# Performance work log

Measured on AMD Instinct MI355X. Metric: run time of the kernel, lower is better.

## Reference

```python
import jax, jax.numpy as jnp
import numpy as np

NHEAD = 16
EPS = 1e-5


def layer_norm(x, w, b):
    mu = jnp.mean(x, axis=-1, keepdims=True)
    var = jnp.var(x, axis=-1, keepdims=True)
    return (x - mu) * jax.lax.rsqrt(var + EPS) * w + b


def setup_inputs() -> dict:
    key = jax.random.key(0)
    ks = jax.random.split(key, 14)
    B, S, E, F = 16, 1024, 1024, 4096
    s = 0.02
    return {
        "x": jax.random.normal(ks[0], (B, S, E), jnp.float32),
        "in_proj_w": jax.random.normal(ks[1], (3 * E, E), jnp.float32) * s,
        "in_proj_b": jax.random.normal(ks[2], (3 * E,), jnp.float32) * s,
        "out_w": jax.random.normal(ks[3], (E, E), jnp.float32) * s,
        "out_b": jax.random.normal(ks[4], (E,), jnp.float32) * s,
        "lin1_w": jax.random.normal(ks[5], (F, E), jnp.float32) * s,
        "lin1_b": jax.random.normal(ks[6], (F,), jnp.float32) * s,
        "lin2_w": jax.random.normal(ks[7], (E, F), jnp.float32) * s,
        "lin2_b": jax.random.normal(ks[8], (E,), jnp.float32) * s,
        "norm1_w": jnp.ones((E,), jnp.float32),
        "norm1_b": jnp.zeros((E,), jnp.float32),
        "norm2_w": jnp.ones((E,), jnp.float32),
        "norm2_b": jnp.zeros((E,), jnp.float32),
    }


def reference(x, in_proj_w, in_proj_b, out_w, out_b, lin1_w, lin1_b, lin2_w, lin2_b,
              norm1_w, norm1_b, norm2_w, norm2_b):
    B, S, E = x.shape
    H = NHEAD
    D = E // H

    # --- pre-norm self-attention (q = k = v = norm1(x)) ---
    xn = layer_norm(x, norm1_w, norm1_b)
    qkv = xn @ in_proj_w.T + in_proj_b                      # [B,S,3E]
    q, k, v = jnp.split(qkv, 3, axis=-1)
    q = q.reshape(B, S, H, D)
    k = k.reshape(B, S, H, D)
    v = v.reshape(B, S, H, D)
    scale = 1.0 / jnp.sqrt(jnp.asarray(D, x.dtype))
    scores = jnp.einsum("bqhd,bkhd->bhqk", q, k) * scale    # [B,H,S,S]
    attn = jax.nn.softmax(scores, axis=-1)
    ctx = jnp.einsum("bhqk,bkhd->bqhd", attn, v).reshape(B, S, E)
    attn_out = ctx @ out_w.T + out_b
    x = x + attn_out

    # --- pre-norm feedforward (gelu) ---
    xn2 = layer_norm(x, norm2_w, norm2_b)
    h = jax.nn.gelu(xn2 @ lin1_w.T + lin1_b, approximate=False)
    x = x + (h @ lin2_w.T + lin2_b)
    return x
```

## Files before the change

kernel.cpp:

```cpp
#include <hip/hip_runtime.h>


typedef __attribute__((ext_vector_type(8))) short bf16x8;
typedef __attribute__((ext_vector_type(4))) float f32x4;
typedef __attribute__((ext_vector_type(8))) unsigned short u16x8;
typedef __attribute__((ext_vector_type(4))) unsigned short u16x4;

__device__ __forceinline__ float bf2f(unsigned short u) {
    return __uint_as_float(((unsigned int)u) << 16);
}
__device__ __forceinline__ unsigned short f2bf(float f) {
    unsigned int u = __float_as_uint(f);
    u += 0x7fffu + ((u >> 16) & 1u);
    return (unsigned short)(u >> 16);
}
__device__ __forceinline__ unsigned int pkbf_trunc(float a, float b) {
    return (__float_as_uint(a) >> 16) | (__float_as_uint(b) & 0xffff0000u);
}

__device__ __forceinline__ void gload_lds16(const unsigned short* g, unsigned short* l) {
    __builtin_amdgcn_global_load_lds(
        (const __attribute__((address_space(1))) unsigned int*)g,
        (__attribute__((address_space(3))) unsigned int*)l, 16, 0, 0);
}

#define FENCE() asm volatile("" ::: "memory")
#define BAR()                         \
    do {                              \
        FENCE();                      \
        __builtin_amdgcn_s_barrier(); \
        FENCE();                      \
    } while (0)
#define VMCNT(n)                                               \
    do {                                                       \
        asm volatile("s_waitcnt vmcnt(" #n ")" ::: "memory");  \
        __builtin_amdgcn_sched_barrier(0);                     \
    } while (0)

__global__ __launch_bounds__(256) void cvt_kernel(const float* __restrict__ in,
                                                  unsigned short* __restrict__ out, int n4) {
    int i = blockIdx.x * 256 + threadIdx.x;
    if (i >= n4) return;
    float4 v = ((const float4*)in)[i];
    u16x4 o;
    o[0] = f2bf(v.x); o[1] = f2bf(v.y); o[2] = f2bf(v.z); o[3] = f2bf(v.w);
    ((u16x4*)out)[i] = o;
}

__global__ __launch_bounds__(256) void ln_kernel(const float* __restrict__ x,
                                                 const float* __restrict__ w,
                                                 const float* __restrict__ b,
                                                 unsigned short* __restrict__ out) {
    const int row = blockIdx.x;
    const int t = threadIdx.x;
    const float* xr = x + (size_t)row * 1024;
    float4 v = *(const float4*)(xr + t * 4);
    float s = v.x + v.y + v.z + v.w;
    float sq = v.x * v.x + v.y * v.y + v.z * v.z + v.w * v.w;
#pragma unroll
    for (int off = 32; off > 0; off >>= 1) {
        s += __shfl_xor(s, off);
        sq += __shfl_xor(sq, off);
    }
    __shared__ float rs_[4], rq_[4];
    if ((t & 63) == 0) { rs_[t >> 6] = s; rq_[t >> 6] = sq; }
    __syncthreads();
    s = rs_[0] + rs_[1] + rs_[2] + rs_[3];
    sq = rq_[0] + rq_[1] + rq_[2] + rq_[3];
    const float mu = s * (1.0f / 1024.0f);
    const float var = sq * (1.0f / 1024.0f) - mu * mu;
    const float rstd = rsqrtf(var + 1e-5f);
    const int c = t * 4;
    float4 wv = *(const float4*)(w + c);
    float4 bv = *(const float4*)(b + c);
    u16x4 o;
    o[0] = f2bf((v.x - mu) * rstd * wv.x + bv.x);
    o[1] = f2bf((v.y - mu) * rstd * wv.y + bv.y);
    o[2] = f2bf((v.z - mu) * rstd * wv.z + bv.z);
    o[3] = f2bf((v.w - mu) * rstd * wv.w + bv.w);
    *(u16x4*)(out + (size_t)row * 1024 + c) = o;
}

template <int EPI>
__global__ __launch_bounds__(512, 2) void gemm_bt(const unsigned short* __restrict__ A,
                                                  const unsigned short* __restrict__ Bt,
                                                  const float* __restrict__ bias,
                                                  const float* __restrict__ resid,
                                                  void* __restrict__ outp,
                                                  int M, int N, int K) {
    __shared__ __align__(16) unsigned short sA[2][256 * 64];
    __shared__ __align__(16) unsigned short sB[2][256 * 64];
    const int t = threadIdx.x;
    const int lane = t & 63;
    const int w = t >> 6;
    const int wm = w >> 2;
    const int wn = w & 3;
    const int quad = lane >> 4;
    const int cl = lane & 15;

    const int nwg = gridDim.x * gridDim.y;
    int wg = blockIdx.y * gridDim.x + blockIdx.x;
    wg = (wg & 7) * (nwg >> 3) + (wg >> 3);
    const int mBase = (wg / gridDim.x) * 256;
    const int nBase = (wg % gridDim.x) * 256;

    const int rl = lane >> 3;
    const int ch = ((lane & 7) ^ rl) * 8;
    const unsigned short* gA = A + (size_t)mBase * K;
    const unsigned short* gB = Bt + (size_t)nBase * K;

#define STAGE_A(buf, hf, k0)                                                          \
    do {                                                                              \
        _Pragma("unroll") for (int u_ = 0; u_ < 2; ++u_) {                            \
            const int r_ = (hf) * 128 + (w * 2 + u_) * 8;                             \
            gload_lds16(gA + (size_t)(r_ + rl) * K + (k0) + ch, &sA[buf][r_ * 64]);   \
        }                                                                             \
    } while (0)
#define STAGE_B(buf, hf, k0)                                                          \
    do {                                                                              \
        _Pragma("unroll") for (int u_ = 0; u_ < 2; ++u_) {                            \
            const int r_ = (hf) * 128 + (w * 2 + u_) * 8;                             \
            gload_lds16(gB + (size_t)(r_ + rl) * K + (k0) + ch, &sB[buf][r_ * 64]);   \
        }                                                                             \
    } while (0)
#define READ_B8(buf)                                                                  \
    do {                                                                              \
        _Pragma("unroll") for (int nf_ = 0; nf_ < 4; ++nf_) {                         \
            const int rb_ = wn * 64 + nf_ * 16 + cl;                                  \
            _Pragma("unroll") for (int ks_ = 0; ks_ < 2; ++ks_)                       \
                bf[nf_][ks_] = *(const bf16x8*)(&sB[buf][rb_ * 64 +                   \
                                     (((quad + 4 * ks_) ^ (rb_ & 7)) * 8)]);          \
        }                                                                             \
    } while (0)
#define READ_A2(buf, mfb)                                                             \
    do {                                                                              \
        _Pragma("unroll") for (int m_ = 0; m_ < 2; ++m_) {                            \
            const int ra_ = wm * 128 + ((mfb) + m_) * 16 + cl;                        \
            _Pragma("unroll") for (int ks_ = 0; ks_ < 2; ++ks_)                       \
                af[m_][ks_] = *(const bf16x8*)(&sA[buf][ra_ * 64 +                    \
                                     (((quad + 4 * ks_) ^ (ra_ & 7)) * 8)]);          \
        }                                                                             \
    } while (0)
#define MFMA_Q(q)                                                                     \
    do {                                                                              \
        __builtin_amdgcn_s_setprio(1);                                                \
        _Pragma("unroll") for (int m_ = 0; m_ < 2; ++m_)                              \
            _Pragma("unroll") for (int nf_ = 0; nf_ < 4; ++nf_)                       \
                _Pragma("unroll") for (int ks_ = 0; ks_ < 2; ++ks_)                   \
                    acc[2 * (q) + m_][nf_] = __builtin_amdgcn_mfma_f32_16x16x32_bf16( \
                        af[m_][ks_], bf[nf_][ks_], acc[2 * (q) + m_][nf_], 0, 0, 0);  \
        __builtin_amdgcn_s_setprio(0);                                                \
    } while (0)

    f32x4 acc[8][4] = {};
    bf16x8 bf[4][2];
    bf16x8 af[2][2];

    STAGE_A(0, 0, 0); STAGE_A(0, 1, 0);
    STAGE_B(0, 0, 0); STAGE_B(0, 1, 0);
    STAGE_B(1, 0, 64); STAGE_B(1, 1, 64);
    VMCNT(4);
    BAR();

    const int NI = K >> 7;
    for (int i = 0; i < NI; ++i) {
        const bool more = (i + 1 < NI);
        const int kT1 = (i << 7) + 64;
        const int kN = (i + 1) << 7;
        READ_B8(0); READ_A2(0, 0);
        STAGE_A(1, 0, kT1);
        BAR(); MFMA_Q(0); BAR();
        READ_A2(0, 2);
        STAGE_A(1, 1, kT1);
        BAR(); MFMA_Q(1); BAR();
        READ_A2(0, 4);
        if (more) STAGE_B(0, 0, kN);
        BAR(); MFMA_Q(2); BAR();
        READ_A2(0, 6);
        if (more) STAGE_B(0, 1, kN);
        BAR(); MFMA_Q(3);
        if (more) { VMCNT(4); } else { VMCNT(0); }
        BAR();
        READ_B8(1); READ_A2(1, 0);
        if (more) STAGE_A(0, 0, kN);
        BAR(); MFMA_Q(0); BAR();
        READ_A2(1, 2);
        if (more) STAGE_A(0, 1, kN);
        BAR(); MFMA_Q(1); BAR();
        READ_A2(1, 4);
        if (more) STAGE_B(1, 0, kN + 64);
        BAR(); MFMA_Q(2); BAR();
        READ_A2(1, 6);
        if (more) STAGE_B(1, 1, kN + 64);
        BAR(); MFMA_Q(3);
        if (more) VMCNT(4);
        BAR();
    }

#pragma unroll
    for (int mf = 0; mf < 8; ++mf) {
        const int rowg = mBase + wm * 128 + mf * 16 + quad * 4;
#pragma unroll
        for (int nf = 0; nf < 4; ++nf) {
            const int colg = nBase + wn * 64 + nf * 16 + cl;
            const float bv = bias[colg];
#pragma unroll
            for (int rr = 0; rr < 4; ++rr) {
                const float v = acc[mf][nf][rr] + bv;
                const size_t idx = (size_t)(rowg + rr) * N + colg;
                if constexpr (EPI == 0) {
                    ((unsigned short*)outp)[idx] = f2bf(v);
                } else if constexpr (EPI == 1) {
                    ((float*)outp)[idx] = v + resid[idx];
                } else {
                    const float g = 0.5f * v * (1.0f + erff(v * 0.70710678118654752f));
                    ((unsigned short*)outp)[idx] = f2bf(g);
                }
            }
        }
    }
#undef STAGE_A
#undef STAGE_B
#undef READ_B8
#undef READ_A2
#undef MFMA_Q
}

__global__ __launch_bounds__(256) void attn_mfma(const unsigned short* __restrict__ qkv,
                                                 unsigned short* __restrict__ ctx) {
    __shared__ __align__(16) unsigned short Ks[64 * 72];
    __shared__ __align__(16) unsigned int Vt[64 * 36];
    __shared__ __align__(16) unsigned short Ps[128 * 72];

    const int bh = blockIdx.x;
    const int qt = blockIdx.y;
    const int b = bh >> 4;
    const int h = bh & 15;
    const int t = threadIdx.x;
    const int w = t >> 6;
    const int lane = t & 63;
    const int quad = lane >> 4;
    const int cl = lane & 15;
    const size_t tok0 = (size_t)b * 1024;
    const int qrow0 = qt * 128 + w * 32;

    bf16x8 aq[2][2];
#pragma unroll
    for (int sub = 0; sub < 2; ++sub) {
        const unsigned short* qp =
            qkv + (tok0 + qrow0 + sub * 16 + cl) * 3072 + h * 64 + quad * 8;
        aq[sub][0] = *(const bf16x8*)(qp);
        aq[sub][1] = *(const bf16x8*)(qp + 32);
    }

    const bf16x8 vones = {0x3F80, 0x3F80, 0x3F80, 0x3F80, 0x3F80, 0x3F80, 0x3F80, 0x3F80};

    const int r0 = t >> 2;
    const int c16 = (t & 3) * 16;
    const int kp = t >> 3;
    const int dc = t & 7;

    f32x4 acc[2][5] = {};
    float m_r[2] = {-3.0e38f, -3.0e38f};

    for (int kt = 0; kt < 16; ++kt) {
        {
            const unsigned short* kg =
                qkv + (tok0 + kt * 64 + r0) * 3072 + 1024 + h * 64 + c16;
            *(int4*)(Ks + r0 * 72 + c16) = *(const int4*)(kg);
            *(int4*)(Ks + r0 * 72 + c16 + 8) = *(const int4*)(kg + 8);

            const unsigned short* vg =
                qkv + (tok0 + kt * 64 + 2 * kp) * 3072 + 2048 + h * 64 + dc * 8;
            u16x8 v0 = *(const u16x8*)(vg);
            u16x8 v1 = *(const u16x8*)(vg + 3072);
            const int g = kp >> 2, wd = kp & 3;
#pragma unroll
            for (int j = 0; j < 8; ++j) {
                const int d = dc * 8 + j;
                Vt[d * 36 + (((g ^ (d >> 3)) << 2) | wd)] =
                    ((unsigned int)v1[j] << 16) | (unsigned int)v0[j];
            }
        }
        __syncthreads();

#pragma unroll
        for (int sub = 0; sub < 2; ++sub) {
            f32x4 sc[4] = {};
#pragma unroll
            for (int i = 0; i < 4; ++i) {
                const int rb = i * 16 + cl;
#pragma unroll
                for (int ks = 0; ks < 2; ++ks) {
                    bf16x8 bk = *(const bf16x8*)(Ks + rb * 72 + quad * 8 + ks * 32);
                    sc[i] = __builtin_amdgcn_mfma_f32_16x16x32_bf16(bk, aq[sub][ks], sc[i],
                                                                    0, 0, 0);
                }
            }
            float mx0 = fmaxf(fmaxf(sc[0][0], sc[0][1]), fmaxf(sc[0][2], sc[0][3]));
            float mx1 = fmaxf(fmaxf(sc[1][0], sc[1][1]), fmaxf(sc[1][2], sc[1][3]));
            float mx2 = fmaxf(fmaxf(sc[2][0], sc[2][1]), fmaxf(sc[2][2], sc[2][3]));
            float mx3 = fmaxf(fmaxf(sc[3][0], sc[3][1]), fmaxf(sc[3][2], sc[3][3]));
            float rmax = fmaxf(fmaxf(mx0, mx1), fmaxf(mx2, mx3));
            rmax = fmaxf(rmax, __shfl_xor(rmax, 16));
            rmax = fmaxf(rmax, __shfl_xor(rmax, 32));
            const float mnew = fmaxf(m_r[sub], rmax * 0.125f);
            const float alpha = __expf(m_r[sub] - mnew);
            m_r[sub] = mnew;
            float al[4];
#pragma unroll
            for (int rr = 0; rr < 4; ++rr) al[rr] = __shfl(alpha, quad * 4 + rr, 16);
#pragma unroll
            for (int j = 0; j < 5; ++j)
#pragma unroll
                for (int rr = 0; rr < 4; ++rr) acc[sub][j][rr] *= al[rr];
            const unsigned short* pr = Ps + (w * 32 + sub * 16 + cl) * 72;
#pragma unroll
            for (int i = 0; i < 4; ++i) {
                const float p0 = __expf(fmaf(sc[i][0], 0.125f, -mnew));
                const float p1 = __expf(fmaf(sc[i][1], 0.125f, -mnew));
                const float p2 = __expf(fmaf(sc[i][2], 0.125f, -mnew));
                const float p3 = __expf(fmaf(sc[i][3], 0.125f, -mnew));
                uint2 pk;
                pk.x = pkbf_trunc(p0, p1);
                pk.y = pkbf_trunc(p2, p3);
                *(uint2*)(pr + i * 16 + quad * 4) = pk;
            }
        }

#pragma unroll
        for (int ks = 0; ks < 2; ++ks) {
            bf16x8 bv[4];
#pragma unroll
            for (int j = 0; j < 4; ++j) {
                const int d = j * 16 + cl;
                bv[j] = *(const bf16x8*)(Vt + d * 36 + (((quad + 4 * ks) ^ (d >> 3)) << 2));
            }
#pragma unroll
            for (int sub = 0; sub < 2; ++sub) {
                bf16x8 ap =
                    *(const bf16x8*)(Ps + (w * 32 + sub * 16 + cl) * 72 + quad * 8 + ks * 32);
#pragma unroll
                for (int j = 0; j < 4; ++j)
                    acc[sub][j] =
                        __builtin_amdgcn_mfma_f32_16x16x32_bf16(ap, bv[j], acc[sub][j], 0, 0, 0);
                acc[sub][4] =
                    __builtin_amdgcn_mfma_f32_16x16x32_bf16(ap, vones, acc[sub][4], 0, 0, 0);
            }
        }
        __syncthreads();
    }

#pragma unroll
    for (int sub = 0; sub < 2; ++sub)
#pragma unroll
        for (int rr = 0; rr < 4; ++rr) {
            const float inv = 1.0f / acc[sub][4][rr];
            const size_t tok = tok0 + qt * 128 + w * 32 + sub * 16 + quad * 4 + rr;
#pragma unroll
            for (int j = 0; j < 4; ++j)
                ctx[tok * 1024 + h * 64 + j * 16 + cl] = f2bf(acc[sub][j][rr] * inv);
        }
}

extern "C" void kernel_launch(void* const* d_in, const int* in_sizes, int n_in,
                              void* d_out, int out_size, void* d_ws, size_t ws_size,
                              hipStream_t stream) {
    const float* x    = (const float*)d_in[0];
    const float* wqkv = (const float*)d_in[1];
    const float* bqkv = (const float*)d_in[2];
    const float* wo   = (const float*)d_in[3];
    const float* bo   = (const float*)d_in[4];
    const float* w1   = (const float*)d_in[5];
    const float* b1   = (const float*)d_in[6];
    const float* w2   = (const float*)d_in[7];
    const float* b2   = (const float*)d_in[8];
    const float* n1w  = (const float*)d_in[9];
    const float* n1b  = (const float*)d_in[10];
    const float* n2w  = (const float*)d_in[11];
    const float* n2b  = (const float*)d_in[12];
    float* out = (float*)d_out;

    char* ws = (char*)d_ws;
    unsigned short* wqkv_b = (unsigned short*)(ws);
    unsigned short* wo_b   = (unsigned short*)(ws + 6291456);
    unsigned short* w1_b   = (unsigned short*)(ws + 8388608);
    unsigned short* w2_b   = (unsigned short*)(ws + 16777216);
    unsigned short* r1     = (unsigned short*)(ws + 25165824);
    unsigned short* r2     = (unsigned short*)(ws + 58720256);

    unsigned short* xn_b  = r1;
    unsigned short* ctx_b = r1;
    unsigned short* xn2_b = r1;
    unsigned short* qkv_b = r2;
    unsigned short* h_b   = r2;

    cvt_kernel<<<3072, 256, 0, stream>>>(wqkv, wqkv_b, 786432);
    cvt_kernel<<<1024, 256, 0, stream>>>(wo, wo_b, 262144);
    cvt_kernel<<<4096, 256, 0, stream>>>(w1, w1_b, 1048576);
    cvt_kernel<<<4096, 256, 0, stream>>>(w2, w2_b, 1048576);

    ln_kernel<<<16384, 256, 0, stream>>>(x, n1w, n1b, xn_b);
    gemm_bt<0><<<dim3(12, 64), 512, 0, stream>>>(xn_b, wqkv_b, bqkv, nullptr, qkv_b,
                                                 16384, 3072, 1024);
    attn_mfma<<<dim3(256, 8), 256, 0, stream>>>(qkv_b, ctx_b);
    gemm_bt<1><<<dim3(4, 64), 512, 0, stream>>>(ctx_b, wo_b, bo, x, out, 16384, 1024, 1024);
    ln_kernel<<<16384, 256, 0, stream>>>(out, n2w, n2b, xn2_b);

    if (ws_size >= 192937984ULL) {
        gemm_bt<2><<<dim3(16, 64), 512, 0, stream>>>(xn2_b, w1_b, b1, nullptr, h_b,
                                                     16384, 4096, 1024);
        gemm_bt<1><<<dim3(4, 64), 512, 0, stream>>>(h_b, w2_b, b2, out, out,
                                                    16384, 1024, 4096);
    } else {
        for (int c = 0; c < 2; ++c) {
            const size_t row0 = (size_t)c * 8192;
            gemm_bt<2><<<dim3(16, 32), 512, 0, stream>>>(xn2_b + row0 * 1024, w1_b, b1,
                                                         nullptr, h_b, 8192, 4096, 1024);
            gemm_bt<1><<<dim3(4, 32), 512, 0, stream>>>(h_b, w2_b, b2, out + row0 * 1024,
                                                        out + row0 * 1024, 8192, 1024, 4096);
        }
    }
}
```

Measured before the change: 873.4 us.

## Make GEMM persistent over multiple tiles with cross-tile prefetch and fast GELU

Turns gemm_bt into a persistent kernel: a fixed grid of 256 workgroups each walks several output tiles. The next tile's K-slabs are prefetched during the current tile's last iterations, so the pipeline does not drain between tiles. The epilogue runs inline once a tile's K loop finishes, and the accumulators are then reset. It also replaces erff in the GELU epilogue with an Abramowitz-Stegun polynomial approximation using rcp and exp, which is cheaper but slightly less accurate.

```diff
diff --git a/kernel.cpp b/kernel.cpp
--- a/kernel.cpp
+++ b/kernel.cpp
@@ -16,6 +16,21 @@
 }
 __device__ __forceinline__ unsigned int pkbf_trunc(float a, float b) {
     return (__float_as_uint(a) >> 16) | (__float_as_uint(b) & 0xffff0000u);
+}
+
+__device__ __forceinline__ float fast_gelu(float v) {
+    const float x = v * 0.70710678118654752f;
+    const float ax = fabsf(x);
+    const float t = __builtin_amdgcn_rcpf(fmaf(0.3275911f, ax, 1.0f));
+    float p = fmaf(1.061405429f, t, -1.453152027f);
+    p = fmaf(p, t, 1.421413741f);
+    p = fmaf(p, t, -0.284496736f);
+    p = fmaf(p, t, 0.254829592f);
+    p = p * t;
+    const float e = __expf(-x * x);
+    float erfv = fmaf(-p, e, 1.0f);
+    erfv = (x < 0.0f) ? -erfv : erfv;
+    return 0.5f * v * (1.0f + erfv);
 }
 
 __device__ __forceinline__ void gload_lds16(const unsigned short* g, unsigned short* l) {
@@ -87,7 +102,7 @@
                                                   const float* __restrict__ bias,
                                                   const float* __restrict__ resid,
                                                   void* __restrict__ outp,
-                                                  int M, int N, int K) {
+                                                  int M, int N, int K, int cnt) {
     __shared__ __align__(16) unsigned short sA[2][256 * 64];
     __shared__ __align__(16) unsigned short sB[2][256 * 64];
     const int t = threadIdx.x;
@@ -98,37 +113,35 @@
     const int quad = lane >> 4;
     const int cl = lane & 15;
 
-    const int nwg = gridDim.x * gridDim.y;
-    int wg = blockIdx.y * gridDim.x + blockIdx.x;
-    wg = (wg & 7) * (nwg >> 3) + (wg >> 3);
-    const int mBase = (wg / gridDim.x) * 256;
-    const int nBase = (wg % gridDim.x) * 256;
+    const int GY = M >> 8;
+    const int nt = GY * (N >> 8);
+    const int NB = gridDim.x;
+    const int g = blockIdx.x;
+
+#define DECODE(gg, mB, nB)                                  \
+    do {                                                    \
+        const int l_ = ((gg) & 7) * (nt >> 3) + ((gg) >> 3);\
+        const int nq_ = l_ / GY;                            \
+        (nB) = nq_ << 8;                                    \
+        (mB) = (l_ - nq_ * GY) << 8;                        \
+    } while (0)
 
     const int rl = lane >> 3;
     const int ch = ((lane & 7) ^ rl) * 8;
-    const unsigned short* gA = A + (size_t)mBase * K;
-    const unsigned short* gB = Bt + (size_t)nBase * K;
-
-#define STAGE_A(buf, hf, k0)                                                          \
-    do {                                                                              \
-        _Pragma("unroll") for (int u_ = 0; u_ < 2; ++u_) {                            \
-            const int r_ = (hf) * 128 + (w * 2 + u_) * 8;                             \
-            gload_lds16(gA + (size_t)(r_ + rl) * K + (k0) + ch, &sA[buf][r_ * 64]);   \
-        }                                                                             \
-    } while (0)
-#define STAGE_B(buf, hf, k0)                                                          \
-    do {                                                                              \
-        _Pragma("unroll") for (int u_ = 0; u_ < 2; ++u_) {                            \
-            const int r_ = (hf) * 128 + (w * 2 + u_) * 8;                             \
-            gload_lds16(gB + (size_t)(r_ + rl) * K + (k0) + ch, &sB[buf][r_ * 64]);   \
-        }                                                                             \
+
+#define STG(gp, sbuf, buf, hf, k0)                                                     \
+    do {                                                                               \
+        _Pragma("unroll") for (int u_ = 0; u_ < 2; ++u_) {                             \
+            const int r_ = (hf) * 128 + (w * 2 + u_) * 8;                              \
+            gload_lds16((gp) + (size_t)(r_ + rl) * K + (k0) + ch, &sbuf[buf][r_ * 64]);\
+        }                                                                              \
     } while (0)
 #define READ_B8(buf)                                                                  \
     do {                                                                              \
         _Pragma("unroll") for (int nf_ = 0; nf_ < 4; ++nf_) {                         \
             const int rb_ = wn * 64 + nf_ * 16 + cl;                                  \
             _Pragma("unroll") for (int ks_ = 0; ks_ < 2; ++ks_)                       \
-                bf[nf_][ks_] = *(const bf16x8*)(&sB[buf][rb_ * 64 +                   \
+                bfr[nf_][ks_] = *(const bf16x8*)(&sB[buf][rb_ * 64 +                  \
                                      (((quad + 4 * ks_) ^ (rb_ & 7)) * 8)]);          \
         }                                                                             \
     } while (0)
@@ -148,82 +161,108 @@
             _Pragma("unroll") for (int nf_ = 0; nf_ < 4; ++nf_)                       \
                 _Pragma("unroll") for (int ks_ = 0; ks_ < 2; ++ks_)                   \
                     acc[2 * (q) + m_][nf_] = __builtin_amdgcn_mfma_f32_16x16x32_bf16( \
-                        af[m_][ks_], bf[nf_][ks_], acc[2 * (q) + m_][nf_], 0, 0, 0);  \
+                        af[m_][ks_], bfr[nf_][ks_], acc[2 * (q) + m_][nf_], 0, 0, 0); \
         __builtin_amdgcn_s_setprio(0);                                                \
     } while (0)
 
     f32x4 acc[8][4] = {};
-    bf16x8 bf[4][2];
+    bf16x8 bfr[4][2];
     bf16x8 af[2][2];
 
-    STAGE_A(0, 0, 0); STAGE_A(0, 1, 0);
-    STAGE_B(0, 0, 0); STAGE_B(0, 1, 0);
-    STAGE_B(1, 0, 64); STAGE_B(1, 1, 64);
+    int mBc, nBc, mBn, nBn;
+    DECODE(g, mBc, nBc);
+    const unsigned short* gAc = A + (size_t)mBc * K;
+    const unsigned short* gBc = Bt + (size_t)nBc * K;
+    int kc = 0;
+    mBn = mBc; nBn = nBc;
+    const unsigned short* gAn = gAc;
+    const unsigned short* gBn = gBc;
+    int kn = 128;
+    int tj = 0;
+
+    STG(gAc, sA, 0, 0, kc); STG(gAc, sA, 0, 1, kc);
+    STG(gBc, sB, 0, 0, kc); STG(gBc, sB, 0, 1, kc);
+    STG(gBc, sB, 1, 0, kc + 64); STG(gBc, sB, 1, 1, kc + 64);
     VMCNT(4);
     BAR();
 
-    const int NI = K >> 7;
-    for (int i = 0; i < NI; ++i) {
-        const bool more = (i + 1 < NI);
-        const int kT1 = (i << 7) + 64;
-        const int kN = (i + 1) << 7;
+    const int TP = cnt * (K >> 7);
+    for (int P = 0; P < TP; ++P) {
+        const bool more = (P + 1 < TP);
         READ_B8(0); READ_A2(0, 0);
-        STAGE_A(1, 0, kT1);
+        STG(gAc, sA, 1, 0, kc + 64);
         BAR(); MFMA_Q(0); BAR();
         READ_A2(0, 2);
-        STAGE_A(1, 1, kT1);
+        STG(gAc, sA, 1, 1, kc + 64);
         BAR(); MFMA_Q(1); BAR();
         READ_A2(0, 4);
-        if (more) STAGE_B(0, 0, kN);
+        if (more) STG(gBn, sB, 0, 0, kn);
         BAR(); MFMA_Q(2); BAR();
         READ_A2(0, 6);
-        if (more) STAGE_B(0, 1, kN);
+        if (more) STG(gBn, sB, 0, 1, kn);
         BAR(); MFMA_Q(3);
         if (more) { VMCNT(4); } else { VMCNT(0); }
         BAR();
         READ_B8(1); READ_A2(1, 0);
-        if (more) STAGE_A(0, 0, kN);
+        if (more) STG(gAn, sA, 0, 0, kn);
         BAR(); MFMA_Q(0); BAR();
         READ_A2(1, 2);
-        if (more) STAGE_A(0, 1, kN);
+        if (more) STG(gAn, sA, 0, 1, kn);
         BAR(); MFMA_Q(1); BAR();
         READ_A2(1, 4);
-        if (more) STAGE_B(1, 0, kN + 64);
+        if (more) STG(gBn, sB, 1, 0, kn + 64);
         BAR(); MFMA_Q(2); BAR();
         READ_A2(1, 6);
-        if (more) STAGE_B(1, 1, kN + 64);
+        if (more) STG(gBn, sB, 1, 1, kn + 64);
         BAR(); MFMA_Q(3);
         if (more) VMCNT(4);
         BAR();
+
+        if (kc + 128 == K) {
+#pragma unroll
+            for (int mf = 0; mf < 8; ++mf) {
+                const int rowg = mBc + wm * 128 + mf * 16 + quad * 4;
+#pragma unroll
+                for (int nf = 0; nf < 4; ++nf) {
+                    const int colg = nBc + wn * 64 + nf * 16 + cl;
+                    const float bv = bias[colg];
+#pragma unroll
+                    for (int rr = 0; rr < 4; ++rr) {
+                        const float v = acc[mf][nf][rr] + bv;
+                        const size_t idx = (size_t)(rowg + rr) * N + colg;
+                        if constexpr (EPI == 0) {
+                            ((unsigned short*)outp)[idx] = f2bf(v);
+                        } else if constexpr (EPI == 1) {
+                            ((float*)outp)[idx] = v + resid[idx];
+                        } else {
+                            ((unsigned short*)outp)[idx] = f2bf(fast_gelu(v));
+                        }
+                    }
+                }
+            }
+            const f32x4 z = {0.f, 0.f, 0.f, 0.f};
+#pragma unroll
+            for (int mf = 0; mf < 8; ++mf)
+#pragma unroll
+                for (int nf = 0; nf < 4; ++nf) acc[mf][nf] = z;
+        }
+        kc = kn; gAc = gAn; gBc = gBn; mBc = mBn; nBc = nBn;
+        kn += 128;
+        if (kn >= K) {
+            kn = 0;
+            ++tj;
+            if (tj < cnt) {
+                DECODE(g + tj * NB, mBn, nBn);
+                gAn = A + (size_t)mBn * K;
+                gBn = Bt + (size_t)nBn * K;
+            }
+        }
     }
-
-#pragma unroll
-    for (int mf = 0; mf < 8; ++mf) {
-        const int rowg = mBase + wm * 128 + mf * 16 + quad * 4;
-#pragma unroll
-        for (int nf = 0; nf < 4; ++nf) {
-            const int colg = nBase + wn * 64 + nf * 16 + cl;
-            const float bv = bias[colg];
-#pragma unroll
-            for (int rr = 0; rr < 4; ++rr) {
-                const float v = acc[mf][nf][rr] + bv;
-                const size_t idx = (size_t)(rowg + rr) * N + colg;
-                if constexpr (EPI == 0) {
-                    ((unsigned short*)outp)[idx] = f2bf(v);
-                } else if constexpr (EPI == 1) {
-                    ((float*)outp)[idx] = v + resid[idx];
-                } else {
-                    const float g = 0.5f * v * (1.0f + erff(v * 0.70710678118654752f));
-                    ((unsigned short*)outp)[idx] = f2bf(g);
-                }
-            }
-        }
-    }
-#undef STAGE_A
-#undef STAGE_B
+#undef STG
 #undef READ_B8
 #undef READ_A2
 #undef MFMA_Q
+#undef DECODE
 }
 
 __global__ __launch_bounds__(256) void attn_mfma(const unsigned short* __restrict__ qkv,
@@ -401,24 +440,24 @@
     cvt_kernel<<<4096, 256, 0, stream>>>(w2, w2_b, 1048576);
 
     ln_kernel<<<16384, 256, 0, stream>>>(x, n1w, n1b, xn_b);
-    gemm_bt<0><<<dim3(12, 64), 512, 0, stream>>>(xn_b, wqkv_b, bqkv, nullptr, qkv_b,
-                                                 16384, 3072, 1024);
+    gemm_bt<0><<<256, 512, 0, stream>>>(xn_b, wqkv_b, bqkv, nullptr, qkv_b,
+                                        16384, 3072, 1024, 3);
     attn_mfma<<<dim3(256, 8), 256, 0, stream>>>(qkv_b, ctx_b);
-    gemm_bt<1><<<dim3(4, 64), 512, 0, stream>>>(ctx_b, wo_b, bo, x, out, 16384, 1024, 1024);
+    gemm_bt<1><<<256, 512, 0, stream>>>(ctx_b, wo_b, bo, x, out, 16384, 1024, 1024, 1);
     ln_kernel<<<16384, 256, 0, stream>>>(out, n2w, n2b, xn2_b);
 
     if (ws_size >= 192937984ULL) {
-        gemm_bt<2><<<dim3(16, 64), 512, 0, stream>>>(xn2_b, w1_b, b1, nullptr, h_b,
-                                                     16384, 4096, 1024);
-        gemm_bt<1><<<dim3(4, 64), 512, 0, stream>>>(h_b, w2_b, b2, out, out,
-                                                    16384, 1024, 4096);
+        gemm_bt<2><<<256, 512, 0, stream>>>(xn2_b, w1_b, b1, nullptr, h_b,
+                                            16384, 4096, 1024, 4);
+        gemm_bt<1><<<256, 512, 0, stream>>>(h_b, w2_b, b2, out, out,
+                                            16384, 1024, 4096, 1);
     } else {
         for (int c = 0; c < 2; ++c) {
             const size_t row0 = (size_t)c * 8192;
-            gemm_bt<2><<<dim3(16, 32), 512, 0, stream>>>(xn2_b + row0 * 1024, w1_b, b1,
-                                                         nullptr, h_b, 8192, 4096, 1024);
-            gemm_bt<1><<<dim3(4, 32), 512, 0, stream>>>(h_b, w2_b, b2, out + row0 * 1024,
-                                                        out + row0 * 1024, 8192, 1024, 4096);
+            gemm_bt<2><<<256, 512, 0, stream>>>(xn2_b + row0 * 1024, w1_b, b1,
+                                                nullptr, h_b, 8192, 4096, 1024, 2);
+            gemm_bt<1><<<128, 512, 0, stream>>>(h_b, w2_b, b2, out + row0 * 1024,
+                                                out + row0 * 1024, 8192, 1024, 4096, 1);
         }
     }
 }
```

Result: no change. 881.4 us (+0.9%).
